# Performance work log

Hardware: AMD Instinct MI355X
Metric: run time of the kernel (lower is better)

Reference implementation:

```python
import jax, jax.numpy as jnp
import numpy as np

D_MODEL = 2048
N_HEADS = 16
HEAD_DIM = D_MODEL // N_HEADS  # 128
MAX_T = 2048
ROPE_BASE = 10000.0


def _rope_tables(head_dim, max_t, base):
    inv = 1.0 / (base ** (np.arange(0, head_dim, 2, dtype=np.float32) / head_dim))
    t = np.arange(max_t, dtype=np.float32)
    fr = np.outer(t, inv)  # (T, head_dim//2)
    return jnp.asarray(np.cos(fr)), jnp.asarray(np.sin(fr))


def setup_inputs() -> dict:
    key = jax.random.key(0)
    k1, k2, k3 = jax.random.split(key, 3)
    B, T = 2, 2048
    x = jax.random.normal(k1, (B, T, D_MODEL), dtype=jnp.float32)
    Wqkv = jax.random.normal(k2, (3 * D_MODEL, D_MODEL), dtype=jnp.float32) * 0.02
    Wout = jax.random.normal(k3, (D_MODEL, D_MODEL), dtype=jnp.float32) * 0.02
    cos, sin = _rope_tables(HEAD_DIM, MAX_T, ROPE_BASE)
    rope_mask = jnp.arange(N_HEADS) < (N_HEADS // 2)  # first 8 heads RoPE, rest NoPE
    return {"x": x, "Wqkv": Wqkv, "Wout": Wout, "cos": cos, "sin": sin, "rope_mask": rope_mask}


def _apply_rope(t, cos, sin):
    # t: (B,H,T,hd); pairs are consecutive elements (x0,x1),(x2,x3),...
    B, H, T, hd = t.shape
    tr = t.reshape(B, H, T, hd // 2, 2)
    c = cos[:T][None, None, :, :]
    s = sin[:T][None, None, :, :]
    re = tr[..., 0] * c - tr[..., 1] * s
    im = tr[..., 0] * s + tr[..., 1] * c
    return jnp.stack([re, im], axis=-1).reshape(B, H, T, hd)


def reference(x, Wqkv, Wout, cos, sin, rope_mask):
    B, T, D = x.shape
    H = rope_mask.shape[0]
    hd = D // H
    qkv = x @ Wqkv.T  # (B,T,3D)
    q, k, v = jnp.split(qkv, 3, axis=-1)
    def heads(a):
        return a.reshape(B, T, H, hd).transpose(0, 2, 1, 3)  # (B,H,T,hd)
    q, k, v = heads(q), heads(k), heads(v)
    m = rope_mask[None, :, None, None]  # broadcast over (B,H,T,hd)
    q = jnp.where(m, _apply_rope(q, cos, sin), q)
    k = jnp.where(m, _apply_rope(k, cos, sin), k)
    scale = 1.0 / jnp.sqrt(jnp.asarray(hd, dtype=q.dtype))
    scores = jnp.einsum('bhtd,bhsd->bhts', q, k) * scale
    causal = jnp.tril(jnp.ones((T, T), dtype=bool))
    scores = jnp.where(causal[None, None], scores, jnp.asarray(-jnp.inf, dtype=scores.dtype))
    p = jax.nn.softmax(scores, axis=-1)
    out = jnp.einsum('bhts,bhsd->bhtd', p, v)
    out = out.transpose(0, 2, 1, 3).reshape(B, T, D)
    return out @ Wout.T
```

## Files before the change

kernel.cpp:

```cpp
#include <hip/hip_runtime.h>
#include <stdint.h>

typedef unsigned short u16;
typedef __attribute__((ext_vector_type(8))) short short8;
typedef __attribute__((ext_vector_type(4))) short s16x4;
typedef __attribute__((ext_vector_type(4))) float f32x4;
typedef __attribute__((ext_vector_type(16))) float f32x16;

__device__ __forceinline__ u16 f2bf(float f) {
  uint32_t x = __float_as_uint(f);
  x += 0x7fff + ((x >> 16) & 1);
  return (u16)(x >> 16);
}
__device__ __forceinline__ float bf2f(u16 u) {
  return __uint_as_float(((uint32_t)u) << 16);
}
__device__ __forceinline__ f32x4 mfma16(short8 a, short8 b, f32x4 c) {
  return __builtin_amdgcn_mfma_f32_16x16x32_bf16(a, b, c, 0, 0, 0);
}
__device__ __forceinline__ f32x16 mfma32(short8 a, short8 b, f32x16 c) {
  return __builtin_amdgcn_mfma_f32_32x32x16_bf16(a, b, c, 0, 0, 0);
}
__device__ __forceinline__ f32x4 mfma16k16(s16x4 a, s16x4 b, f32x4 c) {
  return __builtin_amdgcn_mfma_f32_16x16x16bf16_1k(a, b, c, 0, 0, 0);
}
__device__ __forceinline__ void gld16(const u16* g, u16* l) {
  __builtin_amdgcn_global_load_lds(
      (const __attribute__((address_space(1))) unsigned int*)g,
      (__attribute__((address_space(3))) unsigned int*)l, 16, 0, 0);
}
__device__ __forceinline__ float exp2a(float x) {
  float r;
  asm("v_exp_f32 %0, %1" : "=v"(r) : "v"(x));
  return r;
}

#define WAIT_VM(n) asm volatile("s_waitcnt vmcnt(" #n ")" ::: "memory")

__global__ __launch_bounds__(256) void cvt_all(const float* __restrict__ x,
                                               const float* __restrict__ wqkv,
                                               const float* __restrict__ wout,
                                               u16* __restrict__ xb,
                                               u16* __restrict__ wqkvb,
                                               u16* __restrict__ woutb) {
  long i = ((long)blockIdx.x * 256 + threadIdx.x) * 8;
  const float* s;
  u16* d;
  long off;
  if (i < 8388608) {
    s = x; d = xb; off = i;
  } else if (i < 20971520) {
    s = wqkv; d = wqkvb; off = i - 8388608;
  } else {
    s = wout; d = woutb; off = i - 20971520;
  }
  f32x4 a = *(const f32x4*)(s + off);
  f32x4 b = *(const f32x4*)(s + off + 4);
  short8 o;
#pragma unroll
  for (int j = 0; j < 4; j++) {
    o[j] = (short)f2bf(a[j]);
    o[j + 4] = (short)f2bf(b[j]);
  }
  *(short8*)(d + off) = o;
}

__global__ __launch_bounds__(512, 4) void gemm_qkv(const u16* __restrict__ A,
                                                   const u16* __restrict__ Bw,
                                                   u16* __restrict__ q3) {
  __shared__ __align__(16) u16 SA[12288];
  __shared__ __align__(16) u16 SB[24576];
  const int id = blockIdx.x;
  const int swz = (id & 7) * 96 + (id >> 3);
  const int by = swz & 31, bx = swz >> 5;
  const int m0 = by * 128, n0 = bx * 256;
  const int t = threadIdx.x, w = t >> 6, lane = t & 63;
  const int quad = lane >> 4, l15 = lane & 15;
  const int wm = w >> 2, wn = w & 3;
  const int rS = t >> 2, pS = t & 3;
  const int cS = (pS - (rS >> 1)) & 3;
  const size_t arowA = (size_t)(m0 + rS) * 2048 + cS * 8;
  const size_t arowB = (size_t)(n0 + rS) * 2048 + cS * 8;

  f32x4 acc[4][4] = {};
  const int pq = ((quad + (l15 >> 1)) & 3) * 8;

#define STAGE(KT, RS_)                                   \
  {                                                      \
    const u16* ga_ = A + arowA + (size_t)(KT) * 32;      \
    gld16(ga_, SA + (RS_)*4096 + t * 8);                 \
    const u16* gb_ = Bw + arowB + (size_t)(KT) * 32;     \
    u16* lb_ = SB + (RS_)*8192 + t * 8;                  \
    gld16(gb_, lb_);                                     \
    gld16(gb_ + (size_t)128 * 2048, lb_ + 4096);         \
  }

#define TILE(RC, RSS, TAU, DO_STAGE, WAIT)                                    \
  {                                                                           \
    const u16* Sa_ = SA + (RC)*4096;                                          \
    const u16* Sb_ = SB + (RC)*8192;                                          \
    if (DO_STAGE) STAGE((TAU) + 2, RSS);                                      \
    short8 af[4], bf[4];                                                      \
    _Pragma("unroll") for (int i = 0; i < 4; i++)                             \
        af[i] = *(const short8*)&Sa_[(wm * 64 + i * 16 + l15) * 32 + pq];     \
    _Pragma("unroll") for (int n = 0; n < 4; n++)                             \
        bf[n] = *(const short8*)&Sb_[(wn * 64 + n * 16 + l15) * 32 + pq];     \
    __builtin_amdgcn_s_setprio(1);                                            \
    _Pragma("unroll") for (int mi = 0; mi < 4; mi++)                          \
      _Pragma("unroll") for (int ni = 0; ni < 4; ni++)                        \
          acc[mi][ni] = mfma16(af[mi], bf[ni], acc[mi][ni]);                  \
    __builtin_amdgcn_s_setprio(0);                                            \
    WAIT;                                                                     \
    __builtin_amdgcn_s_barrier();                                             \
  }

  STAGE(0, 0);
  STAGE(1, 1);
  WAIT_VM(3);
  __builtin_amdgcn_s_barrier();

#pragma unroll 1
  for (int kt = 0; kt < 60; kt += 3) {
    TILE(0, 2, kt + 0, 1, WAIT_VM(3));
    TILE(1, 0, kt + 1, 1, WAIT_VM(3));
    TILE(2, 1, kt + 2, 1, WAIT_VM(3));
  }
  TILE(0, 2, 60, 1, WAIT_VM(3));
  TILE(1, 0, 61, 1, WAIT_VM(3));
  TILE(2, 1, 62, 0, WAIT_VM(0));
  TILE(0, 2, 63, 0, (void)0);
#undef TILE
#undef STAGE

  const int which = n0 >> 11;
  const int bb = m0 >> 11, tt0 = m0 & 2047;
  if (which == 2) {
    u16* vbase = q3 + 16777216;
#pragma unroll
    for (int ni = 0; ni < 4; ni++) {
      const int gcol = (n0 & 2047) + wn * 64 + ni * 16 + l15;
      const int hh = gcol >> 7, di = gcol & 127;
      u16* vb = vbase + ((size_t)(bb * 16 + hh) * 128 + di) * 2048;
#pragma unroll
      for (int mi = 0; mi < 4; mi++) {
        const int tloc = tt0 + wm * 64 + mi * 16 + quad * 4;
        s16x4 st;
#pragma unroll
        for (int r = 0; r < 4; r++) st[r] = (short)f2bf(acc[mi][ni][r]);
        *(s16x4*)(vb + tloc) = st;
      }
    }
  } else {
    const float sc = (which == 0) ? 0.1275174f : 1.0f;
    u16* base = q3 + (size_t)which * 8388608;
#pragma unroll
    for (int ni = 0; ni < 4; ni++) {
      const int gcol = (n0 & 2047) + wn * 64 + ni * 16 + l15;
      const int hh = gcol >> 7, di = gcol & 127;
      u16* qb = base + ((size_t)(bb * 16 + hh) * 2048) * 128 + di;
#pragma unroll
      for (int mi = 0; mi < 4; mi++) {
        const int tloc = tt0 + wm * 64 + mi * 16 + quad * 4;
#pragma unroll
        for (int r = 0; r < 4; r++)
          qb[(size_t)(tloc + r) * 128] = f2bf(acc[mi][ni][r] * sc);
      }
    }
  }
}

template <int EPI>
__global__ __launch_bounds__(256) void gemm_bt(const u16* __restrict__ A,
                                               const u16* __restrict__ B,
                                               int K, void* __restrict__ Cv, int N) {
  __shared__ __align__(16) u16 SMEM[8448];
  u16* As = SMEM;
  u16* Bs = SMEM + 4096;
  const int m0 = blockIdx.y * 128, n0 = blockIdx.x * 128;
  const int t = threadIdx.x, w = t >> 6, lane = t & 63;
  const int l31 = lane & 31, half = lane >> 5;
  const int rb = (w >> 1) * 64, cb = (w & 1) * 64;
  f32x16 acc[2][2] = {};
  const int rowS = w * 16 + (lane >> 2);
  const int cS = ((lane & 3) - (rowS >> 1)) & 3;
  const u16* ag = A + (size_t)(m0 + rowS) * K + cS * 8;
  const u16* bg = B + (size_t)(n0 + rowS) * K + cS * 8;
  u16* al = As + w * 512 + lane * 8;
  u16* bl = Bs + w * 512 + lane * 8;
  const size_t rowskip = (size_t)64 * K;
  const int p0 = ((0 * 2 + half + (l31 >> 1)) & 3) * 8;
  const int p1 = ((1 * 2 + half + (l31 >> 1)) & 3) * 8;
  for (int k0 = 0; k0 < K; k0 += 32) {
    __syncthreads();
    gld16(ag, al);
    gld16(ag + rowskip, al + 2048);
    gld16(bg, bl);
    gld16(bg + rowskip, bl + 2048);
    ag += 32;
    bg += 32;
    __syncthreads();
    short8 af[2][2], bfr[2][2];
#pragma unroll
    for (int mi = 0; mi < 2; mi++) {
      af[mi][0] = *(const short8*)&As[(rb + mi * 32 + l31) * 32 + p0];
      af[mi][1] = *(const short8*)&As[(rb + mi * 32 + l31) * 32 + p1];
    }
#pragma unroll
    for (int ni = 0; ni < 2; ni++) {
      bfr[ni][0] = *(const short8*)&Bs[(cb + ni * 32 + l31) * 32 + p0];
      bfr[ni][1] = *(const short8*)&Bs[(cb + ni * 32 + l31) * 32 + p1];
    }
#pragma unroll
    for (int kh = 0; kh < 2; kh++)
#pragma unroll
      for (int mi = 0; mi < 2; mi++)
#pragma unroll
        for (int ni = 0; ni < 2; ni++)
          acc[mi][ni] = mfma32(af[mi][kh], bfr[ni][kh], acc[mi][ni]);
  }

  if (EPI == 0) {
    const int which = n0 >> 11;
    const int hh = (n0 & 2047) >> 7;
    const int bb = m0 >> 11, tt0 = m0 & 2047;
    u16* q3 = (u16*)Cv;
    if (which == 2) {
      u16* vbase = q3 + 16777216 + ((size_t)(bb * 16 + hh) * 128) * 2048;
#pragma unroll
      for (int mi = 0; mi < 2; mi++)
#pragma unroll
        for (int ni = 0; ni < 2; ni++) {
          int di = cb + ni * 32 + l31;
          int trow = tt0 + rb + mi * 32 + half * 4;
#pragma unroll
          for (int rg2 = 0; rg2 < 4; rg2++) {
            s16x4 st;
#pragma unroll
            for (int j = 0; j < 4; j++) st[j] = (short)f2bf(acc[mi][ni][rg2 * 4 + j]);
            *(s16x4*)(vbase + (size_t)di * 2048 + trow + rg2 * 8) = st;
          }
        }
    } else {
      const float sc = (which == 0) ? 0.1275174f : 1.0f;
      u16* base = q3 + (size_t)which * 8388608 + ((size_t)(bb * 16 + hh) * 2048) * 128;
#pragma unroll
      for (int mi = 0; mi < 2; mi++)
#pragma unroll
        for (int ni = 0; ni < 2; ni++) {
          int di = cb + ni * 32 + l31;
          int trow = tt0 + rb + mi * 32 + half * 4;
#pragma unroll
          for (int reg = 0; reg < 16; reg++) {
            int tt = trow + (reg & 3) + 8 * (reg >> 2);
            base[(size_t)tt * 128 + di] = f2bf(acc[mi][ni][reg] * sc);
          }
        }
    }
  } else {
    float* Es = (float*)SMEM;
    float* C = (float*)Cv;
#pragma unroll
    for (int r = 0; r < 4; r++) {
      __syncthreads();
      if ((w >> 1) == (r >> 1)) {
        const int mi = r & 1;
#pragma unroll
        for (int ni = 0; ni < 2; ni++) {
          int col = cb + ni * 32 + l31;
#pragma unroll
          for (int reg = 0; reg < 16; reg++) {
            int lrow = (reg & 3) + 8 * (reg >> 2) + half * 4;
            Es[lrow * 132 + col] = acc[mi][ni][reg];
          }
        }
      }
      __syncthreads();
#pragma unroll
      for (int it = 0; it < 4; it++) {
        int idx = it * 256 + t;
        int row = idx >> 5, ch = idx & 31;
        f32x4 vv = *(const f32x4*)&Es[row * 132 + ch * 4];
        *(f32x4*)&C[(size_t)(m0 + r * 32 + row) * N + n0 + ch * 4] = vv;
      }
    }
  }
}

__global__ __launch_bounds__(256) void rope_k(u16* __restrict__ q, u16* __restrict__ k,
                                              const float* __restrict__ cosT,
                                              const float* __restrict__ sinT) {
  int t = threadIdx.x;
  int row = blockIdx.x * 4 + (t >> 6);
  int i = t & 63;
  int b = row >> 14;
  int h = (row >> 11) & 7;
  int tp = row & 2047;
  size_t base = ((size_t)((b * 16 + h) * 2048 + tp)) * 128 + 2 * i;
  float c = cosT[tp * 64 + i], s = sinT[tp * 64 + i];
  {
    uint32_t u = *(uint32_t*)(q + base);
    float x0 = bf2f((u16)(u & 0xffff)), x1 = bf2f((u16)(u >> 16));
    float re = x0 * c - x1 * s, im = x0 * s + x1 * c;
    *(uint32_t*)(q + base) = (uint32_t)f2bf(re) | ((uint32_t)f2bf(im) << 16);
  }
  {
    uint32_t u = *(uint32_t*)(k + base);
    float x0 = bf2f((u16)(u & 0xffff)), x1 = bf2f((u16)(u >> 16));
    float re = x0 * c - x1 * s, im = x0 * s + x1 * c;
    *(uint32_t*)(k + base) = (uint32_t)f2bf(re) | ((uint32_t)f2bf(im) << 16);
  }
}

__global__ __launch_bounds__(256, 2) void attn_k(const u16* __restrict__ qh,
                                                 const u16* __restrict__ kh,
                                                 const u16* __restrict__ vTh,
                                                 u16* __restrict__ attno) {
  __shared__ __align__(16) u16 Ks[8192];
  __shared__ __align__(16) u16 Vt[8192];
  const int i = blockIdx.x;
  const int jj = i & 255, half = i >> 8;
  const int bh = jj >> 3, t8 = jj & 7;
  const int qt = half ? (15 - t8) : t8;
  const int q0 = qt * 128;
  const int t = threadIdx.x, w = t >> 6, lane = t & 63;
  const int quad = lane >> 4, l15 = lane & 15;
  const size_t bhoff = (size_t)bh * 262144;

  short8 qb[2][4];
  {
    const u16* qp = qh + bhoff + (size_t)(q0 + w * 32 + l15) * 128 + quad * 8;
#pragma unroll
    for (int qq = 0; qq < 2; qq++)
#pragma unroll
      for (int ks = 0; ks < 4; ks++)
        qb[qq][ks] = *(const short8*)(qp + qq * 2048 + ks * 32);
  }
  f32x4 of[2][8] = {};
  float mst[2] = {-1e30f, -1e30f}, lst[2] = {0.f, 0.f};
  const int nkt = 2 * qt + 2;
  const int wq0 = q0 + w * 32;

  for (int kt = 0; kt < nkt; kt++) {
    const int k0 = kt * 64;
    __syncthreads();
    {
#pragma unroll
      for (int it = 0; it < 4; it++) {
        int L = it * 256 + t;
        int key = L >> 4, c = L & 15;
        gld16(kh + bhoff + (size_t)(k0 + key) * 128 + ((c ^ (key & 15)) * 8),
              Ks + (size_t)L * 8);
      }
#pragma unroll
      for (int it = 0; it < 4; it++) {
        int L = it * 256 + t;
        int d = L >> 3, c = L & 7;
        gld16(vTh + bhoff + (size_t)d * 2048 + k0 + ((c ^ (d & 7)) * 8),
              Vt + (size_t)L * 8);
      }
    }
    __syncthreads();
    if (k0 <= wq0 + 31) {
      f32x4 sacc[2][4];
#pragma unroll
      for (int qq = 0; qq < 2; qq++)
#pragma unroll
        for (int kk = 0; kk < 4; kk++) sacc[qq][kk] = (f32x4){0.f, 0.f, 0.f, 0.f};
#pragma unroll
      for (int kk = 0; kk < 4; kk++) {
        short8 kf[4];
#pragma unroll
        for (int ks = 0; ks < 4; ks++)
          kf[ks] = *(const short8*)&Ks[(kk * 16 + l15) * 128 + ((ks * 4 + quad) ^ l15) * 8];
#pragma unroll
        for (int qq = 0; qq < 2; qq++)
#pragma unroll
          for (int ks = 0; ks < 4; ks++)
            sacc[qq][kk] = mfma16(kf[ks], qb[qq][ks], sacc[qq][kk]);
      }
      const bool needmask = (k0 + 63 > wq0);
      s16x4 pf[2][4];
      float alpha[2];
#pragma unroll
      for (int qq = 0; qq < 2; qq++) {
        const int qg = wq0 + qq * 16 + l15;
        if (needmask) {
#pragma unroll
          for (int kk = 0; kk < 4; kk++)
#pragma unroll
            for (int rg = 0; rg < 4; rg++)
              if (k0 + kk * 16 + quad * 4 + rg > qg) sacc[qq][kk][rg] = -1e30f;
        }
        float pm = -1e30f;
#pragma unroll
        for (int kk = 0; kk < 4; kk++)
#pragma unroll
          for (int rg = 0; rg < 4; rg++) pm = fmaxf(pm, sacc[qq][kk][rg]);
        pm = fmaxf(pm, __shfl_xor(pm, 16));
        pm = fmaxf(pm, __shfl_xor(pm, 32));
        float mnew = fmaxf(mst[qq], pm);
        alpha[qq] = exp2a(mst[qq] - mnew);
        mst[qq] = mnew;
        float ps = 0.f;
#pragma unroll
        for (int kk = 0; kk < 4; kk++) {
          float e0 = exp2a(sacc[qq][kk][0] - mnew);
          float e1 = exp2a(sacc[qq][kk][1] - mnew);
          float e2 = exp2a(sacc[qq][kk][2] - mnew);
          float e3 = exp2a(sacc[qq][kk][3] - mnew);
          ps += (e0 + e1) + (e2 + e3);
          pf[qq][kk][0] = (short)f2bf(e0);
          pf[qq][kk][1] = (short)f2bf(e1);
          pf[qq][kk][2] = (short)f2bf(e2);
          pf[qq][kk][3] = (short)f2bf(e3);
        }
        ps += __shfl_xor(ps, 16);
        ps += __shfl_xor(ps, 32);
        lst[qq] = lst[qq] * alpha[qq] + ps;
      }
#pragma unroll
      for (int qq = 0; qq < 2; qq++) {
        if (!__all(alpha[qq] == 1.0f)) {
          float a = alpha[qq];
#pragma unroll
          for (int df = 0; df < 8; df++) of[qq][df] *= a;
        }
      }
#pragma unroll
      for (int df = 0; df < 8; df++) {
        s16x4 vf[4];
#pragma unroll
        for (int kk = 0; kk < 4; kk++)
          vf[kk] = *(const s16x4*)&Vt[(df * 16 + l15) * 64 +
                                      ((kk * 2 + (quad >> 1)) ^ (l15 & 7)) * 8 +
                                      (quad & 1) * 4];
#pragma unroll
        for (int qq = 0; qq < 2; qq++)
#pragma unroll
          for (int kk = 0; kk < 4; kk++)
            of[qq][df] = mfma16k16(vf[kk], pf[qq][kk], of[qq][df]);
      }
    }
  }
  const int b = bh >> 4, h = bh & 15;
#pragma unroll
  for (int qq = 0; qq < 2; qq++) {
    float linv = 1.0f / lst[qq];
    const size_t row = (size_t)(b * 2048 + q0 + w * 32 + qq * 16 + l15);
#pragma unroll
    for (int df = 0; df < 8; df++) {
      s16x4 o;
#pragma unroll
      for (int rg = 0; rg < 4; rg++) o[rg] = (short)f2bf(of[qq][df][rg] * linv);
      *(s16x4*)(attno + row * 2048 + h * 128 + df * 16 + quad * 4) = o;
    }
  }
}

extern "C" void kernel_launch(void* const* d_in, const int* in_sizes, int n_in,
                              void* d_out, int out_size, void* d_ws, size_t ws_size,
                              hipStream_t stream) {
  const float* x = (const float*)d_in[0];
  const float* Wqkv = (const float*)d_in[1];
  const float* Wout = (const float*)d_in[2];
  const float* cosT = (const float*)d_in[3];
  const float* sinT = (const float*)d_in[4];
  float* out = (float*)d_out;
  char* ws = (char*)d_ws;
  u16* qkvh = (u16*)(ws + 0);
  u16* woutb = (u16*)(ws + 50331648);
  u16* xb = (u16*)(ws + 58720256);
  u16* wqkvb = (u16*)(ws + 75497472);
  u16* attno = wqkvb;

  cvt_all<<<12288, 256, 0, stream>>>(x, Wqkv, Wout, xb, wqkvb, woutb);
  gemm_qkv<<<768, 512, 0, stream>>>(xb, wqkvb, qkvh);
  rope_k<<<8192, 256, 0, stream>>>(qkvh, qkvh + 8388608, cosT, sinT);
  attn_k<<<512, 256, 0, stream>>>(qkvh, qkvh + 8388608, qkvh + 16777216, attno);
  gemm_bt<1><<<dim3(16, 32), 256, 0, stream>>>(attno, woutb, 2048, (void*)out, 2048);
}
```

Before: 395.2 us.

## Double-buffer K/V tiles in attention kernel and raise MFMA wave priority

Result: no change. 394.9 us (-0.1%).

```diff
diff --git a/kernel.cpp b/kernel.cpp
--- a/kernel.cpp
+++ b/kernel.cpp
@@ -315,8 +315,8 @@
                                                  const u16* __restrict__ kh,
                                                  const u16* __restrict__ vTh,
                                                  u16* __restrict__ attno) {
-  __shared__ __align__(16) u16 Ks[8192];
-  __shared__ __align__(16) u16 Vt[8192];
+  __shared__ __align__(16) u16 Ks[16384];
+  __shared__ __align__(16) u16 Vt[16384];
   const int i = blockIdx.x;
   const int jj = i & 255, half = i >> 8;
   const int bh = jj >> 3, t8 = jj & 7;
@@ -340,27 +340,39 @@
   const int nkt = 2 * qt + 2;
   const int wq0 = q0 + w * 32;
 
+#define ASTAGE(KT, BUF)                                                        \
+  {                                                                            \
+    const int k0_ = (KT) * 64;                                                 \
+    _Pragma("unroll") for (int it = 0; it < 4; it++) {                         \
+      int L = it * 256 + t;                                                    \
+      int key = L >> 4, c = L & 15;                                            \
+      gld16(kh + bhoff + (size_t)(k0_ + key) * 128 + ((c ^ (key & 15)) * 8),   \
+            Ks + (BUF)*8192 + (size_t)L * 8);                                  \
+    }                                                                          \
+    _Pragma("unroll") for (int it = 0; it < 4; it++) {                         \
+      int L = it * 256 + t;                                                    \
+      int d = L >> 3, c = L & 7;                                               \
+      gld16(vTh + bhoff + (size_t)d * 2048 + k0_ + ((c ^ (d & 7)) * 8),        \
+            Vt + (BUF)*8192 + (size_t)L * 8);                                  \
+    }                                                                          \
+  }
+
+  ASTAGE(0, 0);
+#pragma unroll 1
   for (int kt = 0; kt < nkt; kt++) {
+    const int buf = kt & 1;
     const int k0 = kt * 64;
-    __syncthreads();
-    {
-#pragma unroll
-      for (int it = 0; it < 4; it++) {
-        int L = it * 256 + t;
-        int key = L >> 4, c = L & 15;
-        gld16(kh + bhoff + (size_t)(k0 + key) * 128 + ((c ^ (key & 15)) * 8),
-              Ks + (size_t)L * 8);
-      }
-#pragma unroll
-      for (int it = 0; it < 4; it++) {
-        int L = it * 256 + t;
-        int d = L >> 3, c = L & 7;
-        gld16(vTh + bhoff + (size_t)d * 2048 + k0 + ((c ^ (d & 7)) * 8),
-              Vt + (size_t)L * 8);
-      }
-    }
-    __syncthreads();
+    __builtin_amdgcn_s_barrier();
+    if (kt + 1 < nkt) {
+      ASTAGE(kt + 1, buf ^ 1);
+      WAIT_VM(8);
+    } else {
+      WAIT_VM(0);
+    }
+    __builtin_amdgcn_s_barrier();
     if (k0 <= wq0 + 31) {
+      const u16* Kb = Ks + buf * 8192;
+      const u16* Vb = Vt + buf * 8192;
       f32x4 sacc[2][4];
 #pragma unroll
       for (int qq = 0; qq < 2; qq++)
@@ -371,12 +383,14 @@
         short8 kf[4];
 #pragma unroll
         for (int ks = 0; ks < 4; ks++)
-          kf[ks] = *(const short8*)&Ks[(kk * 16 + l15) * 128 + ((ks * 4 + quad) ^ l15) * 8];
+          kf[ks] = *(const short8*)&Kb[(kk * 16 + l15) * 128 + ((ks * 4 + quad) ^ l15) * 8];
+        __builtin_amdgcn_s_setprio(1);
 #pragma unroll
         for (int qq = 0; qq < 2; qq++)
 #pragma unroll
           for (int ks = 0; ks < 4; ks++)
             sacc[qq][kk] = mfma16(kf[ks], qb[qq][ks], sacc[qq][kk]);
+        __builtin_amdgcn_s_setprio(0);
       }
       const bool needmask = (k0 + 63 > wq0);
       s16x4 pf[2][4];
@@ -431,17 +445,20 @@
         s16x4 vf[4];
 #pragma unroll
         for (int kk = 0; kk < 4; kk++)
-          vf[kk] = *(const s16x4*)&Vt[(df * 16 + l15) * 64 +
+          vf[kk] = *(const s16x4*)&Vb[(df * 16 + l15) * 64 +
                                       ((kk * 2 + (quad >> 1)) ^ (l15 & 7)) * 8 +
                                       (quad & 1) * 4];
+        __builtin_amdgcn_s_setprio(1);
 #pragma unroll
         for (int qq = 0; qq < 2; qq++)
 #pragma unroll
           for (int kk = 0; kk < 4; kk++)
             of[qq][df] = mfma16k16(vf[kk], pf[qq][kk], of[qq][df]);
-      }
-    }
-  }
+        __builtin_amdgcn_s_setprio(0);
+      }
+    }
+  }
+#undef ASTAGE
   const int b = bh >> 4, h = bh & 15;
 #pragma unroll
   for (int qq = 0; qq < 2; qq++) {
```
